# Performance work log

Hardware: AMD Instinct MI355X
Metric: run time of the kernel (lower is better)

The kernel has to match this reference:

```python
import jax, jax.numpy as jnp
import numpy as np

SEQ, BATCH, HIDDEN = 2048, 2, 2048
NUM_HEADS = 16
HEAD_DIM = HIDDEN // NUM_HEADS  # 128


def setup_inputs() -> dict:
    key = jax.random.key(0)
    k1, k2, k3, k4, k5 = jax.random.split(key, 5)
    scale = 1.0 / np.sqrt(HIDDEN)
    return {
        "hidden_states": jax.random.normal(k1, (SEQ, BATCH, HIDDEN), dtype=jnp.float32),
        "w_qkv": jax.random.normal(k2, (3 * HIDDEN, HIDDEN), dtype=jnp.float32) * scale,
        "b_qkv": jax.random.normal(k3, (3 * HIDDEN,), dtype=jnp.float32) * 0.01,
        "w_dense": jax.random.normal(k4, (HIDDEN, HIDDEN), dtype=jnp.float32) * scale,
        "b_dense": jax.random.normal(k5, (HIDDEN,), dtype=jnp.float32) * 0.01,
    }


def reference(hidden_states, w_qkv, b_qkv, w_dense, b_dense):
    s, b, H = hidden_states.shape
    nh, d = NUM_HEADS, HEAD_DIM
    norm_factor = jnp.asarray(np.sqrt(d), dtype=hidden_states.dtype)

    # QKV projection: [s, b, 3H] -> [s, b, nh, 3d] -> chunk into q, k, v
    mixed = hidden_states @ w_qkv.T + b_qkv
    mixed = mixed.reshape(s, b, nh, 3 * d)
    q, k, v = jnp.split(mixed, 3, axis=-1)  # each [s, b, nh, d]

    # Causal scaled dot-product attention, materializing [b, nh, sq, sk]
    scores = jnp.einsum("sbhd,tbhd->bhst", q, k) / norm_factor
    causal = jnp.tril(jnp.ones((s, s), dtype=bool))  # [sq, sk]
    scores = jnp.where(causal[None, None, :, :], scores, jnp.asarray(-10000.0, scores.dtype))
    probs = jax.nn.softmax(scores, axis=-1)

    # Context: [s, b, nh, d] -> [s, b, H]
    ctx = jnp.einsum("bhst,tbhd->sbhd", probs, v).reshape(s, b, H)

    # Output projection
    return ctx @ w_dense.T + b_dense
```

## Files before the change

### kernel.cpp

```cpp
#include <hip/hip_runtime.h>
#include <stdint.h>
#include <stddef.h>

#define SEQ   2048
#define BATCH 2
#define HID   2048
#define NH    16
#define HD    128
#define MTOT  (SEQ*BATCH)
#define NQKV  (3*HID)
#define KDIM  HID
#define LOG2E 1.4426950408889634f

#define BK64    64
#define NT64    (KDIM/BK64)

typedef short  bf16x8 __attribute__((ext_vector_type(8)));
typedef float  f32x4  __attribute__((ext_vector_type(4)));

__device__ __forceinline__ unsigned short f2bf(float f) {
  union { float f; uint32_t u; } a; a.f = f;
  uint32_t r = a.u + 0x7fffu + ((a.u >> 16) & 1u);
  return (unsigned short)(r >> 16);
}

__device__ __forceinline__ f32x4 mfma16(bf16x8 a, bf16x8 b, f32x4 c) {
  return __builtin_amdgcn_mfma_f32_16x16x32_bf16(a, b, c, 0, 0, 0);
}

__device__ __forceinline__ void gl_lds16(const unsigned short* g, unsigned short* l) {
  __builtin_amdgcn_global_load_lds(
      (const __attribute__((address_space(1))) void*)g,
      (__attribute__((address_space(3))) void*)l, 16, 0, 0);
}

__global__ void cvt3_f32_bf16(const float* __restrict__ a, unsigned short* __restrict__ oa, int na,
                              const float* __restrict__ b, unsigned short* __restrict__ ob, int nb,
                              const float* __restrict__ c, unsigned short* __restrict__ oc, int nc) {
  int i = blockIdx.x * blockDim.x + threadIdx.x;
  int stride = gridDim.x * blockDim.x;
  int ntot = na + nb + nc;
  for (; i < ntot; i += stride) {
    const float* src; unsigned short* dst; int j;
    if (i < na)           { src = a; dst = oa; j = i; }
    else if (i < na + nb) { src = b; dst = ob; j = i - na; }
    else                  { src = c; dst = oc; j = i - na - nb; }
    float4 f = reinterpret_cast<const float4*>(src)[j];
    ushort4 o;
    o.x = f2bf(f.x); o.y = f2bf(f.y); o.z = f2bf(f.z); o.w = f2bf(f.w);
    reinterpret_cast<ushort4*>(dst)[j] = o;
  }
}


#define QBUFS 28672

#define QSTA(R) gl_lds16(Asrc + (size_t)(R) * KDIM + koff, &db[((R) + w * 8) * 64])
#define QSTB(R) gl_lds16(Bsrc + (size_t)(R) * KDIM + koff, &db[16384 + ((R) + w * 8) * 64])
#define QSTAGE7 do { QSTB(0); QSTB(64); QSTB(128);                            \
                     QSTA(0); QSTA(64); QSTA(128); QSTA(192); } while (0)

#define RD_A4v(R, G, SB) do {                                                 \
    R[0] = *(const bf16x8*)&(SB)[abase + (2*(G)    ) * 1024 + ga0];           \
    R[1] = *(const bf16x8*)&(SB)[abase + (2*(G)    ) * 1024 + ga1];           \
    R[2] = *(const bf16x8*)&(SB)[abase + (2*(G) + 1) * 1024 + ga0];           \
    R[3] = *(const bf16x8*)&(SB)[abase + (2*(G) + 1) * 1024 + ga1];           \
  } while (0)

#define RD_B6v(BQ, SB) do {                                                   \
    BQ[0] = *(const bf16x8*)&(SB)[bbase + 0 * 1024 + ga0];                    \
    BQ[1] = *(const bf16x8*)&(SB)[bbase + 1 * 1024 + ga0];                    \
    BQ[2] = *(const bf16x8*)&(SB)[bbase + 2 * 1024 + ga0];                    \
    BQ[3] = *(const bf16x8*)&(SB)[bbase + 0 * 1024 + ga1];                    \
    BQ[4] = *(const bf16x8*)&(SB)[bbase + 1 * 1024 + ga1];                    \
    BQ[5] = *(const bf16x8*)&(SB)[bbase + 2 * 1024 + ga1];                    \
  } while (0)

#define MFMA_G(G, R, BQ) do {                                                 \
    _Pragma("unroll")                                                         \
    for (int n_ = 0; n_ < 3; ++n_) {                                          \
      acc[2*(G)][n_]     = mfma16(R[0], BQ[n_],     acc[2*(G)][n_]);          \
      acc[2*(G)][n_]     = mfma16(R[1], BQ[n_ + 3], acc[2*(G)][n_]);          \
      acc[2*(G) + 1][n_] = mfma16(R[2], BQ[n_],     acc[2*(G) + 1][n_]);      \
      acc[2*(G) + 1][n_] = mfma16(R[3], BQ[n_ + 3], acc[2*(G) + 1][n_]);      \
    }                                                                         \
  } while (0)

#define QTILE_FF(SB, DOSTAGE) do {                                            \
    bf16x8 bq[6], aP[4], aQ[4];                                               \
    RD_B6v(bq, SB);                                                           \
    RD_A4v(aP, 0, SB);                                                        \
    RD_A4v(aQ, 1, SB);                                                        \
    if (DOSTAGE) QSTAGE7;                                                     \
    MFMA_G(0, aP, bq);                                                        \
    RD_A4v(aP, 2, SB);                                                        \
    MFMA_G(1, aQ, bq);                                                        \
    RD_A4v(aQ, 3, SB);                                                        \
    MFMA_G(2, aP, bq);                                                        \
    MFMA_G(3, aQ, bq);                                                        \
    asm volatile("s_waitcnt lgkmcnt(0)" ::: "memory");                        \
    asm volatile("s_waitcnt vmcnt(0)" ::: "memory");                          \
    asm volatile("s_barrier" ::: "memory");                                   \
  } while (0)

__global__ __launch_bounds__(512, 2) void qkv_gemm(
    const unsigned short* __restrict__ A,
    const unsigned short* __restrict__ B,
    const float* __restrict__ bias,
    unsigned short* __restrict__ Qo,
    unsigned short* __restrict__ Ko,
    unsigned short* __restrict__ Vt)
{
  __shared__ unsigned short smb[2 * QBUFS];
  const int id  = blockIdx.x;
  const int swz = (id & 7) * 64 + (id >> 3);
  const int m0 = (swz >> 5) * 256, n0 = (swz & 31) * 192;
  const int t = threadIdx.x, l = t & 63, w = t >> 6;
  const int wm = w >> 2, wn = w & 3;
  const int fr = l & 15, fg = l >> 4;
  const int abase = (wm * 128 + fr) * 64;
  const int bbase = 16384 + (wn * 48 + fr) * 64;
  const int ga0 = ((fg     ) ^ (fr & 7)) * 8;
  const int ga1 = ((fg + 4 ) ^ (fr & 7)) * 8;
  const int srcrow = w * 8 + (l >> 3);
  const int sgr    = ((l & 7) ^ (l >> 3)) * 8;
  const unsigned short* Asrc = A + (size_t)(m0 + srcrow) * KDIM + sgr;
  const unsigned short* Bsrc = B + (size_t)(n0 + srcrow) * KDIM + sgr;

  f32x4 acc[8][3] = {};

  {
    unsigned short* db = smb;
    size_t koff = 0;
    QSTAGE7;
  }
  asm volatile("s_waitcnt vmcnt(0)" ::: "memory");
  asm volatile("s_barrier" ::: "memory");

#pragma unroll 1
  for (int kt = 0; kt < NT64; ++kt) {
    const unsigned short* sb = &smb[(kt & 1) * QBUFS];
    unsigned short* db = &smb[((kt + 1) & 1) * QBUFS];
    size_t koff = (size_t)(kt + 1) * BK64;
    QTILE_FF(sb, (kt < NT64 - 1));
  }

#pragma unroll
  for (int n = 0; n < 3; ++n) {
    int ncol = n0 + wn * 48 + n * 16 + fr;
    float bv = bias[ncol];
    int head = ncol / 384;
    int rem  = ncol - head * 384;
    int wi   = rem >> 7;
    int d    = rem & 127;
#pragma unroll
    for (int m = 0; m < 8; ++m) {
#pragma unroll
      for (int j = 0; j < 4; ++j) {
        int r = m0 + wm * 128 + m * 16 + fg * 4 + j;
        int s = r >> 1, bb = r & 1;
        float val = acc[m][n][j] + bv;
        if (wi == 0) {
          val *= 0.08838834764831845f;
          Qo[(((size_t)(bb * NH + head)) * SEQ + s) * HD + d] = f2bf(val);
        } else if (wi == 1) {
          Ko[(((size_t)(bb * NH + head)) * SEQ + s) * HD + d] = f2bf(val);
        } else {
          Vt[(((size_t)(bb * NH + head)) * HD + d) * SEQ + s] = f2bf(val);
        }
      }
    }
  }
}


#define DBUFS 24576

#define DSTAGE6 do {                                                          \
    gl_lds16(Aw + koff,                    &db[(w * 4 + 0) * 512]);           \
    gl_lds16(Aw + koff + 8  * KDIM,        &db[(w * 4 + 1) * 512]);           \
    gl_lds16(Aw + koff + 16 * KDIM,        &db[(w * 4 + 2) * 512]);           \
    gl_lds16(Aw + koff + 24 * KDIM,        &db[(w * 4 + 3) * 512]);           \
    gl_lds16(Bw + koff,                    &db[16384 + (w * 2 + 0) * 512]);   \
    gl_lds16(Bw + koff + 8 * KDIM,         &db[16384 + (w * 2 + 1) * 512]);   \
  } while (0)

#define MFMA_D(X, Y, M) do {                                                  \
    _Pragma("unroll")                                                         \
    for (int n_ = 0; n_ < 4; ++n_) {                                          \
      acc[M][n_] = mfma16(X, bg0[n_], acc[M][n_]);                            \
      acc[M][n_] = mfma16(Y, bg1[n_], acc[M][n_]);                            \
    }                                                                         \
  } while (0)

#define DTILE_FF(SB, DOSTAGE) do {                                            \
    bf16x8 bg0[4], bg1[4], e0, e1, o0, o1;                                    \
    _Pragma("unroll")                                                         \
    for (int n_ = 0; n_ < 4; ++n_) {                                          \
      bg0[n_] = *(const bf16x8*)&(SB)[b0 + n_ * 1024];                        \
      bg1[n_] = *(const bf16x8*)&(SB)[b1 + n_ * 1024];                        \
    }                                                                         \
    e0 = *(const bf16x8*)&(SB)[a0];                                           \
    e1 = *(const bf16x8*)&(SB)[a1];                                           \
    o0 = *(const bf16x8*)&(SB)[a0 + 1024];                                    \
    o1 = *(const bf16x8*)&(SB)[a1 + 1024];                                    \
    if (DOSTAGE) DSTAGE6;                                                     \
    MFMA_D(e0, e1, 0);                                                        \
    e0 = *(const bf16x8*)&(SB)[a0 + 2048];                                    \
    e1 = *(const bf16x8*)&(SB)[a1 + 2048];                                    \
    MFMA_D(o0, o1, 1);                                                        \
    o0 = *(const bf16x8*)&(SB)[a0 + 3072];                                    \
    o1 = *(const bf16x8*)&(SB)[a1 + 3072];                                    \
    MFMA_D(e0, e1, 2);                                                        \
    MFMA_D(o0, o1, 3);                                                        \
    asm volatile("s_waitcnt lgkmcnt(0)" ::: "memory");                        \
    asm volatile("s_waitcnt vmcnt(0)" ::: "memory");                          \
    asm volatile("s_barrier" ::: "memory");                                   \
  } while (0)

__global__ __launch_bounds__(512, 1) void dense_gemm(
    const unsigned short* __restrict__ A,
    const unsigned short* __restrict__ B,
    const float* __restrict__ bias,
    float* __restrict__ out)
{
  __shared__ unsigned short smd[2 * DBUFS];
  int id  = blockIdx.x;
  int swz = (id & 7) * (gridDim.x >> 3) + (id >> 3);
  const int m0 = (swz / 16) * 256, n0 = (swz % 16) * 128;
  const int t = threadIdx.x, l = t & 63, w = t >> 6;
  const int wm = w >> 1, wn = w & 1;
  const int fr = l & 15, fg = l >> 4;
  const int fx = fr & 7;
  const int srow = l >> 3;
  const int sgr  = ((l & 7) ^ srow) * 8;
  const unsigned short* Aw = A + (size_t)(m0 + w * 32 + srow) * KDIM + sgr;
  const unsigned short* Bw = B + (size_t)(n0 + w * 16 + srow) * KDIM + sgr;
  const int a0 = (wm * 64 + fr) * 64 + ((fg ^ fx) * 8);
  const int a1 = (wm * 64 + fr) * 64 + (((4 + fg) ^ fx) * 8);
  const int b0 = 16384 + (wn * 64 + fr) * 64 + ((fg ^ fx) * 8);
  const int b1 = 16384 + (wn * 64 + fr) * 64 + (((4 + fg) ^ fx) * 8);
  f32x4 acc[4][4] = {};

  {
    unsigned short* db = smd;
    size_t koff = 0;
    DSTAGE6;
  }
  asm volatile("s_waitcnt vmcnt(0)" ::: "memory");
  asm volatile("s_barrier" ::: "memory");

#pragma unroll 1
  for (int kt = 0; kt < NT64; ++kt) {
    const unsigned short* sb = &smd[(kt & 1) * DBUFS];
    unsigned short* db = &smd[((kt + 1) & 1) * DBUFS];
    size_t koff = (size_t)(kt + 1) * BK64;
    DTILE_FF(sb, (kt < NT64 - 1));
  }

  const int g4 = fg * 4;
#pragma unroll
  for (int n = 0; n < 4; ++n) {
    int ncol = n0 + wn * 64 + n * 16 + fr;
    float bv = bias[ncol];
#pragma unroll
    for (int m = 0; m < 4; ++m) {
#pragma unroll
      for (int j = 0; j < 4; ++j) {
        int r = m0 + wm * 64 + m * 16 + g4 + j;
        out[(size_t)r * HID + ncol] = acc[m][n][j] + bv;
      }
    }
  }
}

__global__ __launch_bounds__(256, 2) void attn_fwd(
    const unsigned short* __restrict__ Q,
    const unsigned short* __restrict__ K,
    const unsigned short* __restrict__ Vt,
    unsigned short* __restrict__ ctx)
{
  __shared__ unsigned short Ksh[2][64 * 128];
  __shared__ unsigned short Vsh[2][128 * 64];
  __shared__ unsigned short Psh[4][16 * 72];
  const int t = threadIdx.x, l = t & 63, w = t >> 6;
  int nwg = gridDim.x * gridDim.y;
  int id  = blockIdx.y * gridDim.x + blockIdx.x;
  int swz = (id & 7) * (nwg >> 3) + (id >> 3);
  const int pair = swz & 15;
  const int bh   = swz >> 4;
  const int qtA = pair, qtB = 31 - pair;
  const int fr = l & 15, fg = l >> 4;
  const size_t base  = (size_t)bh * SEQ * HD;
  const size_t vbase = (size_t)bh * HD * SEQ;

#define STAGE(BUF, KT) do {                                                   \
    const unsigned short* Kt_ = K + base + (size_t)((KT) * 64) * HD;          \
    _Pragma("unroll")                                                         \
    for (int i_ = 0; i_ < 4; ++i_) {                                          \
      int ch_  = w * 4 + i_;                                                  \
      int row_ = ch_ * 4 + (l >> 4);                                          \
      int c16_ = (l & 15) ^ (row_ & 7);                                       \
      gl_lds16(Kt_ + (size_t)row_ * HD + c16_ * 8, &Ksh[BUF][ch_ * 512]);     \
    }                                                                         \
    const unsigned short* Vg_ = Vt + vbase + (KT) * 64;                       \
    _Pragma("unroll")                                                         \
    for (int i_ = 0; i_ < 4; ++i_) {                                          \
      int ch_  = w * 4 + i_;                                                  \
      int row_ = ch_ * 8 + (l >> 3);                                          \
      int c16_ = (l & 7) ^ (row_ & 7);                                        \
      gl_lds16(Vg_ + (size_t)row_ * SEQ + c16_ * 8, &Vsh[BUF][ch_ * 512]);    \
    }                                                                         \
  } while (0)

#define COMPUTE_TILE(QF, OACC, MROW, LROW, QT) do {                           \
    f32x4 sacc[4] = {};                                                       \
    _Pragma("unroll")                                                         \
    for (int c_ = 0; c_ < 4; ++c_) {                                          \
      _Pragma("unroll")                                                       \
      for (int n_ = 0; n_ < 4; ++n_) {                                        \
        int krow = n_ * 16 + fr;                                              \
        int g_   = (c_ * 4 + fg) ^ (krow & 7);                                \
        bf16x8 kf = *(const bf16x8*)&Ksh[buf][krow * 128 + g_ * 8];           \
        sacc[n_] = mfma16(QF[c_], kf, sacc[n_]);                              \
      }                                                                       \
    }                                                                         \
    if (kt == (QT)) {                                                         \
      _Pragma("unroll")                                                       \
      for (int n_ = 0; n_ < 4; ++n_)                                          \
        _Pragma("unroll")                                                     \
        for (int j_ = 0; j_ < 4; ++j_)                                        \
          if (n_ * 16 + fr > w * 16 + fg * 4 + j_) sacc[n_][j_] = -1e30f;     \
    }                                                                         \
    float tm_[4];                                                             \
    _Pragma("unroll")                                                         \
    for (int j_ = 0; j_ < 4; ++j_) {                                          \
      float v0 = fmaxf(fmaxf(sacc[0][j_], sacc[1][j_]),                       \
                       fmaxf(sacc[2][j_], sacc[3][j_]));                      \
      v0 = fmaxf(v0, __shfl_xor(v0, 1));                                      \
      v0 = fmaxf(v0, __shfl_xor(v0, 2));                                      \
      v0 = fmaxf(v0, __shfl_xor(v0, 4));                                      \
      v0 = fmaxf(v0, __shfl_xor(v0, 8));                                      \
      tm_[j_] = v0;                                                           \
    }                                                                         \
    float sc_[4], ps_[4];                                                     \
    _Pragma("unroll")                                                         \
    for (int j_ = 0; j_ < 4; ++j_) {                                          \
      float mn_ = fmaxf(MROW[j_], tm_[j_]);                                   \
      sc_[j_] = exp2f((MROW[j_] - mn_) * LOG2E);                              \
      MROW[j_] = mn_;                                                         \
      ps_[j_] = 0.f;                                                          \
    }                                                                         \
    _Pragma("unroll")                                                         \
    for (int n_ = 0; n_ < 4; ++n_)                                            \
      _Pragma("unroll")                                                       \
      for (int j_ = 0; j_ < 4; ++j_) {                                        \
        float p_ = exp2f((sacc[n_][j_] - MROW[j_]) * LOG2E);                  \
        sacc[n_][j_] = p_;                                                    \
        ps_[j_] += p_;                                                        \
      }                                                                       \
    _Pragma("unroll")                                                         \
    for (int j_ = 0; j_ < 4; ++j_) {                                          \
      float s_ = ps_[j_];                                                     \
      s_ += __shfl_xor(s_, 1);                                                \
      s_ += __shfl_xor(s_, 2);                                                \
      s_ += __shfl_xor(s_, 4);                                                \
      s_ += __shfl_xor(s_, 8);                                                \
      LROW[j_] = LROW[j_] * sc_[j_] + s_;                                     \
    }                                                                         \
    _Pragma("unroll")                                                         \
    for (int n_ = 0; n_ < 8; ++n_)                                            \
      _Pragma("unroll")                                                       \
      for (int j_ = 0; j_ < 4; ++j_)                                          \
        OACC[n_][j_] *= sc_[j_];                                              \
    _Pragma("unroll")                                                         \
    for (int n_ = 0; n_ < 4; ++n_)                                            \
      _Pragma("unroll")                                                       \
      for (int j_ = 0; j_ < 4; ++j_)                                          \
        Psh[w][(fg * 4 + j_) * 72 + n_ * 16 + fr] = f2bf(sacc[n_][j_]);       \
    _Pragma("unroll")                                                         \
    for (int ks_ = 0; ks_ < 2; ++ks_) {                                       \
      bf16x8 pf = *(const bf16x8*)&Psh[w][fr * 72 + ks_ * 32 + fg * 8];       \
      _Pragma("unroll")                                                       \
      for (int n_ = 0; n_ < 8; ++n_) {                                        \
        int vrow = n_ * 16 + fr;                                              \
        int g_   = (ks_ * 4 + fg) ^ (vrow & 7);                               \
        bf16x8 vf = *(const bf16x8*)&Vsh[buf][vrow * 64 + g_ * 8];            \
        OACC[n_] = mfma16(pf, vf, OACC[n_]);                                  \
      }                                                                       \
    }                                                                         \
  } while (0)

  bf16x8 qfA[4], qfB[4];
  {
    const unsigned short* qpA = Q + base + (size_t)(qtA * 64 + w * 16 + fr) * HD + fg * 8;
    const unsigned short* qpB = Q + base + (size_t)(qtB * 64 + w * 16 + fr) * HD + fg * 8;
#pragma unroll
    for (int c = 0; c < 4; ++c) {
      qfA[c] = *(const bf16x8*)(qpA + c * 32);
      qfB[c] = *(const bf16x8*)(qpB + c * 32);
    }
  }
  f32x4 oaccA[8] = {}, oaccB[8] = {};
  float mA[4] = {-1e30f, -1e30f, -1e30f, -1e30f};
  float mB[4] = {-1e30f, -1e30f, -1e30f, -1e30f};
  float lA[4] = {0.f, 0.f, 0.f, 0.f};
  float lB[4] = {0.f, 0.f, 0.f, 0.f};

  STAGE(0, 0);
  __syncthreads();
  int buf = 0;
  for (int kt = 0; kt <= qtB; ++kt) {
    if (kt < qtB) STAGE(buf ^ 1, kt + 1);
    COMPUTE_TILE(qfB, oaccB, mB, lB, qtB);
    if (kt <= qtA) COMPUTE_TILE(qfA, oaccA, mA, lA, qtA);
    __syncthreads();
    buf ^= 1;
  }

  const int bb = bh >> 4, h = bh & 15;
#define WRITE_CTX(OACC, LROW, QT) do {                                        \
    _Pragma("unroll")                                                         \
    for (int n_ = 0; n_ < 8; ++n_)                                            \
      _Pragma("unroll")                                                       \
      for (int j_ = 0; j_ < 4; ++j_) {                                        \
        int qrow = (QT) * 64 + w * 16 + fg * 4 + j_;                          \
        float val = OACC[n_][j_] / LROW[j_];                                  \
        ctx[((size_t)(qrow * BATCH + bb)) * HID + h * HD + n_ * 16 + fr] =    \
            f2bf(val);                                                        \
      }                                                                       \
  } while (0)
  WRITE_CTX(oaccA, lA, qtA);
  WRITE_CTX(oaccB, lB, qtB);
#undef STAGE
#undef COMPUTE_TILE
#undef WRITE_CTX
}

extern "C" void kernel_launch(void* const* d_in, const int* in_sizes, int n_in,
                              void* d_out, int out_size, void* d_ws, size_t ws_size,
                              hipStream_t stream) {
  const float* hs      = (const float*)d_in[0];
  const float* w_qkv   = (const float*)d_in[1];
  const float* b_qkv   = (const float*)d_in[2];
  const float* w_dense = (const float*)d_in[3];
  const float* b_dense = (const float*)d_in[4];
  float* out = (float*)d_out;

  unsigned short* hsb = (unsigned short*)d_ws;
  unsigned short* wqb = hsb + (size_t)MTOT * HID;
  unsigned short* wdb = wqb + (size_t)NQKV * HID;
  unsigned short* q   = wdb + (size_t)HID * HID;
  unsigned short* k   = q   + (size_t)MTOT * HID;
  unsigned short* vt  = k   + (size_t)MTOT * HID;
  unsigned short* ctx = vt  + (size_t)MTOT * HID;

  cvt3_f32_bf16<<<2048, 256, 0, stream>>>(
      hs, hsb, (MTOT * HID) / 4,
      w_qkv, wqb, (NQKV * HID) / 4,
      w_dense, wdb, (HID * HID) / 4);

  qkv_gemm<<<dim3((MTOT / 256) * (NQKV / 192)), 512, 0, stream>>>(hsb, wqb, b_qkv, q, k, vt);
  attn_fwd<<<dim3(16, 32), 256, 0, stream>>>(q, k, vt, ctx);
  dense_gemm<<<dim3((MTOT / 256) * (HID / 128)), 512, 0, stream>>>(ctx, wdb, b_dense, out);
}
```

Measured before the change: 276.6 us.

## Restructure QKV GEMM to 256x256 tiles with four-phase interleaved load/MFMA pipeline

The QKV projection GEMM moves from 256x192 to 256x256 output tiles, giving 384 blocks at one block per CU. Each k-tile is split into four phases that interleave LDS fragment reads, partial global-to-LDS staging, and MFMA bursts under raised wave priority. Fine-grained vmcnt waits replace the full drain at the end of each tile. This aims to raise arithmetic intensity and overlap memory with compute, at the cost of more barriers per tile and halved occupancy.

```diff
diff --git a/kernel.cpp b/kernel.cpp
--- a/kernel.cpp
+++ b/kernel.cpp
@@ -53,57 +53,47 @@
 }
 
 
-#define QBUFS 28672
+#define QBUF2 32768
 
 #define QSTA(R) gl_lds16(Asrc + (size_t)(R) * KDIM + koff, &db[((R) + w * 8) * 64])
 #define QSTB(R) gl_lds16(Bsrc + (size_t)(R) * KDIM + koff, &db[16384 + ((R) + w * 8) * 64])
-#define QSTAGE7 do { QSTB(0); QSTB(64); QSTB(128);                            \
-                     QSTA(0); QSTA(64); QSTA(128); QSTA(192); } while (0)
-
-#define RD_A4v(R, G, SB) do {                                                 \
-    R[0] = *(const bf16x8*)&(SB)[abase + (2*(G)    ) * 1024 + ga0];           \
-    R[1] = *(const bf16x8*)&(SB)[abase + (2*(G)    ) * 1024 + ga1];           \
-    R[2] = *(const bf16x8*)&(SB)[abase + (2*(G) + 1) * 1024 + ga0];           \
-    R[3] = *(const bf16x8*)&(SB)[abase + (2*(G) + 1) * 1024 + ga1];           \
-  } while (0)
-
-#define RD_B6v(BQ, SB) do {                                                   \
-    BQ[0] = *(const bf16x8*)&(SB)[bbase + 0 * 1024 + ga0];                    \
-    BQ[1] = *(const bf16x8*)&(SB)[bbase + 1 * 1024 + ga0];                    \
-    BQ[2] = *(const bf16x8*)&(SB)[bbase + 2 * 1024 + ga0];                    \
-    BQ[3] = *(const bf16x8*)&(SB)[bbase + 0 * 1024 + ga1];                    \
-    BQ[4] = *(const bf16x8*)&(SB)[bbase + 1 * 1024 + ga1];                    \
-    BQ[5] = *(const bf16x8*)&(SB)[bbase + 2 * 1024 + ga1];                    \
-  } while (0)
-
-#define MFMA_G(G, R, BQ) do {                                                 \
-    _Pragma("unroll")                                                         \
-    for (int n_ = 0; n_ < 3; ++n_) {                                          \
-      acc[2*(G)][n_]     = mfma16(R[0], BQ[n_],     acc[2*(G)][n_]);          \
-      acc[2*(G)][n_]     = mfma16(R[1], BQ[n_ + 3], acc[2*(G)][n_]);          \
-      acc[2*(G) + 1][n_] = mfma16(R[2], BQ[n_],     acc[2*(G) + 1][n_]);      \
-      acc[2*(G) + 1][n_] = mfma16(R[3], BQ[n_ + 3], acc[2*(G) + 1][n_]);      \
-    }                                                                         \
-  } while (0)
-
-#define QTILE_FF(SB, DOSTAGE) do {                                            \
-    bf16x8 bq[6], aP[4], aQ[4];                                               \
-    RD_B6v(bq, SB);                                                           \
-    RD_A4v(aP, 0, SB);                                                        \
-    RD_A4v(aQ, 1, SB);                                                        \
-    if (DOSTAGE) QSTAGE7;                                                     \
-    MFMA_G(0, aP, bq);                                                        \
-    RD_A4v(aP, 2, SB);                                                        \
-    MFMA_G(1, aQ, bq);                                                        \
-    RD_A4v(aQ, 3, SB);                                                        \
-    MFMA_G(2, aP, bq);                                                        \
-    MFMA_G(3, aQ, bq);                                                        \
+
+#define RD_A4q(MH, GA, SB) do {                                               \
+    aF[0] = *(const bf16x8*)&(SB)[abase + ((MH) * 4 + 0) * 1024 + (GA)];      \
+    aF[1] = *(const bf16x8*)&(SB)[abase + ((MH) * 4 + 1) * 1024 + (GA)];      \
+    aF[2] = *(const bf16x8*)&(SB)[abase + ((MH) * 4 + 2) * 1024 + (GA)];      \
+    aF[3] = *(const bf16x8*)&(SB)[abase + ((MH) * 4 + 3) * 1024 + (GA)];      \
+  } while (0)
+
+#define RD_B4q(GA, SB) do {                                                   \
+    bF[0] = *(const bf16x8*)&(SB)[bbase + 0 * 1024 + (GA)];                   \
+    bF[1] = *(const bf16x8*)&(SB)[bbase + 1 * 1024 + (GA)];                   \
+    bF[2] = *(const bf16x8*)&(SB)[bbase + 2 * 1024 + (GA)];                   \
+    bF[3] = *(const bf16x8*)&(SB)[bbase + 3 * 1024 + (GA)];                   \
+  } while (0)
+
+#define QPH(MH, RDOP, STOP, VMOP) do {                                        \
+    RDOP;                                                                     \
+    STOP;                                                                     \
+    VMOP;                                                                     \
+    asm volatile("s_barrier" ::: "memory");                                   \
     asm volatile("s_waitcnt lgkmcnt(0)" ::: "memory");                        \
-    asm volatile("s_waitcnt vmcnt(0)" ::: "memory");                          \
+    __builtin_amdgcn_sched_barrier(0);                                        \
+    __builtin_amdgcn_s_setprio(1);                                            \
+    _Pragma("unroll")                                                         \
+    for (int m_ = 0; m_ < 4; ++m_)                                            \
+      _Pragma("unroll")                                                       \
+      for (int n_ = 0; n_ < 4; ++n_)                                          \
+        acc[(MH) * 4 + m_][n_] = mfma16(aF[m_], bF[n_], acc[(MH) * 4 + m_][n_]); \
+    __builtin_amdgcn_sched_barrier(0);                                        \
+    __builtin_amdgcn_s_setprio(0);                                            \
     asm volatile("s_barrier" ::: "memory");                                   \
   } while (0)
 
-__global__ __launch_bounds__(512, 2) void qkv_gemm(
+#define VMC2 asm volatile("s_waitcnt vmcnt(2)" ::: "memory")
+#define VMC0 asm volatile("s_waitcnt vmcnt(0)" ::: "memory")
+
+__global__ __launch_bounds__(512, 1) void qkv_gemm(
     const unsigned short* __restrict__ A,
     const unsigned short* __restrict__ B,
     const float* __restrict__ bias,
@@ -111,43 +101,55 @@
     unsigned short* __restrict__ Ko,
     unsigned short* __restrict__ Vt)
 {
-  __shared__ unsigned short smb[2 * QBUFS];
+  __shared__ unsigned short smb[2 * QBUF2];
   const int id  = blockIdx.x;
-  const int swz = (id & 7) * 64 + (id >> 3);
-  const int m0 = (swz >> 5) * 256, n0 = (swz & 31) * 192;
+  const int swz = (id & 7) * 48 + (id >> 3);
+  const int m0 = (swz / 24) * 256, n0 = (swz % 24) * 256;
   const int t = threadIdx.x, l = t & 63, w = t >> 6;
   const int wm = w >> 2, wn = w & 3;
   const int fr = l & 15, fg = l >> 4;
   const int abase = (wm * 128 + fr) * 64;
-  const int bbase = 16384 + (wn * 48 + fr) * 64;
-  const int ga0 = ((fg     ) ^ (fr & 7)) * 8;
-  const int ga1 = ((fg + 4 ) ^ (fr & 7)) * 8;
+  const int bbase = 16384 + (wn * 64 + fr) * 64;
+  const int ga0 = ((fg    ) ^ (fr & 7)) * 8;
+  const int ga1 = ((fg + 4) ^ (fr & 7)) * 8;
   const int srcrow = w * 8 + (l >> 3);
   const int sgr    = ((l & 7) ^ (l >> 3)) * 8;
   const unsigned short* Asrc = A + (size_t)(m0 + srcrow) * KDIM + sgr;
   const unsigned short* Bsrc = B + (size_t)(n0 + srcrow) * KDIM + sgr;
 
-  f32x4 acc[8][3] = {};
+  f32x4 acc[8][4] = {};
+  bf16x8 aF[4], bF[4];
 
   {
     unsigned short* db = smb;
     size_t koff = 0;
-    QSTAGE7;
-  }
-  asm volatile("s_waitcnt vmcnt(0)" ::: "memory");
+    QSTB(0); QSTB(64); QSTB(128); QSTB(192);
+    QSTA(0); QSTA(128); QSTA(64); QSTA(192);
+  }
+  VMC2;
   asm volatile("s_barrier" ::: "memory");
 
 #pragma unroll 1
-  for (int kt = 0; kt < NT64; ++kt) {
-    const unsigned short* sb = &smb[(kt & 1) * QBUFS];
-    unsigned short* db = &smb[((kt + 1) & 1) * QBUFS];
+  for (int kt = 0; kt < NT64 - 1; ++kt) {
+    const unsigned short* sb = &smb[(kt & 1) * QBUF2];
+    unsigned short* db = &smb[((kt + 1) & 1) * QBUF2];
     size_t koff = (size_t)(kt + 1) * BK64;
-    QTILE_FF(sb, (kt < NT64 - 1));
-  }
-
-#pragma unroll
-  for (int n = 0; n < 3; ++n) {
-    int ncol = n0 + wn * 48 + n * 16 + fr;
+    QPH(0, RD_B4q(ga0, sb); RD_A4q(0, ga0, sb), QSTB(0);   QSTB(64),  VMC2);
+    QPH(1, RD_A4q(1, ga0, sb),                  QSTB(128); QSTB(192), (void)0);
+    QPH(0, RD_B4q(ga1, sb); RD_A4q(0, ga1, sb), QSTA(0);   QSTA(128), (void)0);
+    QPH(1, RD_A4q(1, ga1, sb),                  QSTA(64);  QSTA(192), VMC2);
+  }
+  {
+    const unsigned short* sb = &smb[((NT64 - 1) & 1) * QBUF2];
+    QPH(0, RD_B4q(ga0, sb); RD_A4q(0, ga0, sb), (void)0, VMC0);
+    QPH(1, RD_A4q(1, ga0, sb),                  (void)0, (void)0);
+    QPH(0, RD_B4q(ga1, sb); RD_A4q(0, ga1, sb), (void)0, (void)0);
+    QPH(1, RD_A4q(1, ga1, sb),                  (void)0, (void)0);
+  }
+
+#pragma unroll
+  for (int n = 0; n < 4; ++n) {
+    int ncol = n0 + wn * 64 + n * 16 + fr;
     float bv = bias[ncol];
     int head = ncol / 384;
     int rem  = ncol - head * 384;
@@ -460,7 +462,7 @@
       w_qkv, wqb, (NQKV * HID) / 4,
       w_dense, wdb, (HID * HID) / 4);
 
-  qkv_gemm<<<dim3((MTOT / 256) * (NQKV / 192)), 512, 0, stream>>>(hsb, wqb, b_qkv, q, k, vt);
+  qkv_gemm<<<dim3((MTOT / 256) * (NQKV / 256)), 512, 0, stream>>>(hsb, wqb, b_qkv, q, k, vt);
   attn_fwd<<<dim3(16, 32), 256, 0, stream>>>(q, k, vt, ctx);
   dense_gemm<<<dim3((MTOT / 256) * (HID / 128)), 512, 0, stream>>>(ctx, wdb, b_dense, out);
 }
```

New measurement: 291.0 us. 1.05x slower.
